# Kernel tuning notes

Hardware: AMD Instinct MI355X
Metric: run time of the kernel (lower is better)

## Reference

```python
import jax, jax.numpy as jnp
import numpy as np

NUM_USERS = 200000
NUM_ITEMS = 200000
D = 64          # embedding_dim
S = 20          # num_sample
N = 100000      # nodes per side
EPS = 1e-12     # torch F.normalize eps


def setup_inputs() -> dict:
    key = jax.random.key(0)
    ks = jax.random.split(key, 14)
    inp = {
        'user_nodes': jax.random.randint(ks[0], (N,), 0, NUM_USERS),
        'item_nodes': jax.random.randint(ks[1], (N,), 0, NUM_ITEMS),
        'user_neighbors': jax.random.randint(ks[2], (N, S), 0, NUM_USERS),
        'item_neighbors': jax.random.randint(ks[3], (N, S), 0, NUM_ITEMS),
        'user_table': 0.01 * jax.random.normal(ks[4], (NUM_USERS, D), jnp.float32),
        'item_table': 0.01 * jax.random.normal(ks[5], (NUM_ITEMS, D), jnp.float32),
        'Wsu': jax.random.normal(ks[6], (D, D), jnp.float32) / np.sqrt(D),
        'bsu': jnp.zeros((D,), jnp.float32),
        'Wnu': jax.random.normal(ks[7], (D, D), jnp.float32) / np.sqrt(D),
        'bnu': jnp.zeros((D,), jnp.float32),
        'Wsi': jax.random.normal(ks[8], (D, D), jnp.float32) / np.sqrt(D),
        'bsi': jnp.zeros((D,), jnp.float32),
        'Wni': jax.random.normal(ks[9], (D, D), jnp.float32) / np.sqrt(D),
        'bni': jnp.zeros((D,), jnp.float32),
    }
    return inp


def _sage_layer(table, nodes, neighbors, Ws, bs, Wn, bn):
    self_e = table[nodes]                        # [N, D] gather
    neigh_agg = jnp.mean(table[neighbors], axis=1)  # [N, S, D] gather -> mean -> [N, D]
    h = jax.nn.relu(self_e @ Ws.T + bs + neigh_agg @ Wn.T + bn)
    # dropout p=0 (eval) -> identity; L2 normalize rows (torch F.normalize)
    norm = jnp.maximum(jnp.linalg.norm(h, axis=1, keepdims=True), EPS)
    return h / norm


def reference(user_nodes, item_nodes, user_neighbors, item_neighbors,
              user_table, item_table,
              Wsu, bsu, Wnu, bnu, Wsi, bsi, Wni, bni):
    user_embs = _sage_layer(user_table, user_nodes, user_neighbors, Wsu, bsu, Wnu, bnu)
    item_embs = _sage_layer(item_table, item_nodes, item_neighbors, Wsi, bsi, Wni, bni)
    return (user_embs, item_embs)
```

## Files before the change

kernel.cpp:

```cpp
#include <hip/hip_runtime.h>

typedef __attribute__((ext_vector_type(8))) short bf16x8;
typedef __attribute__((ext_vector_type(4))) float f32x4;

#define DD 64
#define SS 20
#define NPW 16
#define NPB 64

#define SWZ(u, w) ((((((w) >> 2)) ^ ((u) & 15)) << 2) | ((w) & 3))

__device__ __forceinline__ unsigned cvt_pk_bf16(float lo, float hi) {
    unsigned r;
    asm("v_cvt_pk_bf16_f32 %0, %1, %2" : "=v"(r) : "v"(lo), "v"(hi));
    return r;
}

__global__ __launch_bounds__(256) void to_bf16(const float* __restrict__ src,
                                               uint* __restrict__ dst, long n8)
{
    const long stride = (long)gridDim.x * blockDim.x;
    for (long i = (long)blockIdx.x * blockDim.x + threadIdx.x; i < n8; i += stride) {
        const float4 a = ((const float4*)src)[2 * i];
        const float4 b = ((const float4*)src)[2 * i + 1];
        uint4 p;
        p.x = cvt_pk_bf16(a.x, a.y);
        p.y = cvt_pk_bf16(a.z, a.w);
        p.z = cvt_pk_bf16(b.x, b.y);
        p.w = cvt_pk_bf16(b.z, b.w);
        ((uint4*)dst)[i] = p;
    }
}

__global__ __launch_bounds__(256, 4) void sage_bf16(
    const int*  __restrict__ u_nodes, const int* __restrict__ i_nodes,
    const int*  __restrict__ u_nbrs,  const int* __restrict__ i_nbrs,
    const uint* __restrict__ u_tb,    const uint* __restrict__ i_tb,
    const float* __restrict__ Wsu, const float* __restrict__ bsu,
    const float* __restrict__ Wnu, const float* __restrict__ bnu,
    const float* __restrict__ Wsi, const float* __restrict__ bsi,
    const float* __restrict__ Wni, const float* __restrict__ bni,
    float* __restrict__ out, int N, int nblk_side)
{
    __shared__ unsigned BP[16 * 64 * 4];
    __shared__ unsigned XW[4][NPW][64];

    const int tid    = threadIdx.x;
    const int lane   = tid & 63;
    const int wid    = tid >> 6;
    const int lane15 = lane & 15;
    const int grp    = lane >> 4;

    const bool item_side = (int)blockIdx.x >= nblk_side;
    const int  blk = item_side ? (int)blockIdx.x - nblk_side : (int)blockIdx.x;

    const int*  nodes = item_side ? i_nodes : u_nodes;
    const int*  nbrs  = item_side ? i_nbrs  : u_nbrs;
    const uint* tb    = item_side ? i_tb    : u_tb;
    const float* Ws   = item_side ? Wsi : Wsu;
    const float* bsp  = item_side ? bsi : bsu;
    const float* Wn   = item_side ? Wni : Wnu;
    const float* bnp  = item_side ? bni : bnu;
    float* o = out + (item_side ? (size_t)N * DD : 0);

    #pragma unroll
    for (int it = 0; it < 4; ++it) {
        const int fid = it * 4 + wid;
        const int t = fid >> 2, c = fid & 3;
        const int n  = c * 16 + lane15;
        const int kb = t * 32 + (grp << 3);
        const float* src = (kb < 64) ? (Ws + n * 64 + kb) : (Wn + n * 64 + (kb - 64));
        const float4 v0 = *(const float4*)(src);
        const float4 v1 = *(const float4*)(src + 4);
        uint4 p;
        p.x = cvt_pk_bf16(v0.x, v0.y);
        p.y = cvt_pk_bf16(v0.z, v0.w);
        p.z = cvt_pk_bf16(v1.x, v1.y);
        p.w = cvt_pk_bf16(v1.z, v1.w);
        *(uint4*)&BP[(fid * 64 + lane) * 4] = p;
    }

    float bcol[4];
    #pragma unroll
    for (int c = 0; c < 4; ++c) {
        const int col = c * 16 + lane15;
        bcol[c] = bsp[col] + bnp[col];
    }
    __syncthreads();

    const int n0 = blk * NPB + wid * NPW;
    if (n0 >= N) return;

    const int nd = nodes[min(n0 + lane15, N - 1)];

    #pragma unroll
    for (int sb = 0; sb < 4; ++sb) {
        const int u  = sb * 4 + grp;
        const int nn = min(n0 + u, N - 1);

        const int  nb0 = nbrs[(size_t)nn * SS + lane15];
        const long f1  = min((long)nn * SS + 16 + lane15, (long)N * SS - 1);
        const int  nb1 = nbrs[f1];

        const int sidx = __shfl(nd, u, 64);
        const uint2 sv = ((const uint2*)(tb + (size_t)sidx * 32))[lane15];

        float a0 = 0.f, a1 = 0.f, a2 = 0.f, a3 = 0.f;
        #pragma unroll
        for (int b = 0; b < SS; ++b) {
            const int idx = (b < 16) ? __shfl(nb0, (lane & 48) | b, 64)
                                     : __shfl(nb1, (lane & 48) | (b - 16), 64);
            const uint2 r = ((const uint2*)(tb + (size_t)idx * 32))[lane15];
            a0 += __uint_as_float(r.x << 16);
            a1 += __uint_as_float(r.x & 0xffff0000u);
            a2 += __uint_as_float(r.y << 16);
            a3 += __uint_as_float(r.y & 0xffff0000u);
        }
        const float is = 1.0f / SS;

        const int m = lane15;
        uint2 pagg;
        pagg.x = cvt_pk_bf16(a0 * is, a1 * is);
        pagg.y = cvt_pk_bf16(a2 * is, a3 * is);
        *(uint2*)&XW[wid][u][SWZ(u, 2 * m)]      = sv;
        *(uint2*)&XW[wid][u][SWZ(u, 32 + 2 * m)] = pagg;
    }

    union AB { uint4 u4; bf16x8 v; };
    const f32x4 zero = {0.f, 0.f, 0.f, 0.f};
    f32x4 acc[4] = {zero, zero, zero, zero};
    #pragma unroll
    for (int t = 0; t < 4; ++t) {
        const int r     = lane15;
        const int chunk = t * 4 + grp;
        AB a;
        a.u4 = *(const uint4*)&XW[wid][r][((chunk ^ r) << 2)];
        #pragma unroll
        for (int c = 0; c < 4; ++c) {
            AB b;
            b.u4 = *(const uint4*)&BP[((t * 4 + c) * 64 + lane) * 4];
            acc[c] = __builtin_amdgcn_mfma_f32_16x16x32_bf16(a.v, b.v, acc[c], 0, 0, 0);
        }
    }

    float rl[4][4];
    float ssq[4] = {0.f, 0.f, 0.f, 0.f};
    #pragma unroll
    for (int c = 0; c < 4; ++c) {
        #pragma unroll
        for (int j = 0; j < 4; ++j) {
            const float v = fmaxf(acc[c][j] + bcol[c], 0.f);
            rl[c][j] = v;
            ssq[j] = fmaf(v, v, ssq[j]);
        }
    }
    #pragma unroll
    for (int j = 0; j < 4; ++j) {
        #pragma unroll
        for (int m = 1; m < 16; m <<= 1)
            ssq[j] += __shfl_xor(ssq[j], m, 64);
    }
    float inv[4];
    #pragma unroll
    for (int j = 0; j < 4; ++j)
        inv[j] = 1.0f / fmaxf(sqrtf(ssq[j]), 1e-12f);

    #pragma unroll
    for (int j = 0; j < 4; ++j) {
        const int row = (grp << 2) + j;
        const int ni  = n0 + row;
        if (ni < N) {
            #pragma unroll
            for (int c = 0; c < 4; ++c)
                o[(size_t)ni * DD + c * 16 + lane15] = rl[c][j] * inv[j];
        }
    }
}

__global__ __launch_bounds__(256, 4) void sage_fp32(
    const int*   __restrict__ u_nodes, const int* __restrict__ i_nodes,
    const int*   __restrict__ u_nbrs,  const int* __restrict__ i_nbrs,
    const float* __restrict__ u_table, const float* __restrict__ i_table,
    const float* __restrict__ Wsu, const float* __restrict__ bsu,
    const float* __restrict__ Wnu, const float* __restrict__ bnu,
    const float* __restrict__ Wsi, const float* __restrict__ bsi,
    const float* __restrict__ Wni, const float* __restrict__ bni,
    float* __restrict__ out, int N, int nblk_side)
{
    __shared__ unsigned BP[16 * 64 * 4];
    __shared__ unsigned XW[4][NPW][64];

    const int tid    = threadIdx.x;
    const int lane   = tid & 63;
    const int wid    = tid >> 6;
    const int lane15 = lane & 15;
    const int grp    = lane >> 4;

    const bool item_side = (int)blockIdx.x >= nblk_side;
    const int  blk = item_side ? (int)blockIdx.x - nblk_side : (int)blockIdx.x;

    const int*   nodes = item_side ? i_nodes : u_nodes;
    const int*   nbrs  = item_side ? i_nbrs  : u_nbrs;
    const float* table = item_side ? i_table : u_table;
    const float* Ws    = item_side ? Wsi : Wsu;
    const float* bsp   = item_side ? bsi : bsu;
    const float* Wn    = item_side ? Wni : Wnu;
    const float* bnp   = item_side ? bni : bnu;
    float* o = out + (item_side ? (size_t)N * DD : 0);

    #pragma unroll
    for (int it = 0; it < 4; ++it) {
        const int fid = it * 4 + wid;
        const int t = fid >> 2, c = fid & 3;
        const int n  = c * 16 + lane15;
        const int kb = t * 32 + (grp << 3);
        const float* src = (kb < 64) ? (Ws + n * 64 + kb) : (Wn + n * 64 + (kb - 64));
        const float4 v0 = *(const float4*)(src);
        const float4 v1 = *(const float4*)(src + 4);
        uint4 p;
        p.x = cvt_pk_bf16(v0.x, v0.y);
        p.y = cvt_pk_bf16(v0.z, v0.w);
        p.z = cvt_pk_bf16(v1.x, v1.y);
        p.w = cvt_pk_bf16(v1.z, v1.w);
        *(uint4*)&BP[(fid * 64 + lane) * 4] = p;
    }

    float bcol[4];
    #pragma unroll
    for (int c = 0; c < 4; ++c) bcol[c] = bsp[c * 16 + lane15] + bnp[c * 16 + lane15];
    __syncthreads();

    const int n0 = blk * NPB + wid * NPW;
    if (n0 >= N) return;

    const int nd = nodes[min(n0 + lane15, N - 1)];

    #pragma unroll
    for (int sb = 0; sb < 4; ++sb) {
        const int u  = sb * 4 + grp;
        const int nn = min(n0 + u, N - 1);
        const int  nb0 = nbrs[(size_t)nn * SS + lane15];
        const long f1  = min((long)nn * SS + 16 + lane15, (long)N * SS - 1);
        const int  nb1 = nbrs[f1];
        const int sidx = __shfl(nd, u, 64);
        const float4 self4 = ((const float4*)(table + (size_t)sidx * DD))[lane15];
        float4 agg = {0.f, 0.f, 0.f, 0.f};
        #pragma unroll
        for (int b = 0; b < SS; ++b) {
            const int idx = (b < 16) ? __shfl(nb0, (lane & 48) | b, 64)
                                     : __shfl(nb1, (lane & 48) | (b - 16), 64);
            const float4 r4 = ((const float4*)(table + (size_t)idx * DD))[lane15];
            agg.x += r4.x; agg.y += r4.y; agg.z += r4.z; agg.w += r4.w;
        }
        const float is = 1.0f / SS;
        const int m = lane15;
        uint2 pself, pagg;
        pself.x = cvt_pk_bf16(self4.x, self4.y);
        pself.y = cvt_pk_bf16(self4.z, self4.w);
        pagg.x  = cvt_pk_bf16(agg.x * is, agg.y * is);
        pagg.y  = cvt_pk_bf16(agg.z * is, agg.w * is);
        *(uint2*)&XW[wid][u][SWZ(u, 2 * m)]      = pself;
        *(uint2*)&XW[wid][u][SWZ(u, 32 + 2 * m)] = pagg;
    }

    union AB { uint4 u4; bf16x8 v; };
    const f32x4 zero = {0.f, 0.f, 0.f, 0.f};
    f32x4 acc[4] = {zero, zero, zero, zero};
    #pragma unroll
    for (int t = 0; t < 4; ++t) {
        const int r     = lane15;
        const int chunk = t * 4 + grp;
        AB a;
        a.u4 = *(const uint4*)&XW[wid][r][((chunk ^ r) << 2)];
        #pragma unroll
        for (int c = 0; c < 4; ++c) {
            AB b;
            b.u4 = *(const uint4*)&BP[((t * 4 + c) * 64 + lane) * 4];
            acc[c] = __builtin_amdgcn_mfma_f32_16x16x32_bf16(a.v, b.v, acc[c], 0, 0, 0);
        }
    }

    float rl[4][4];
    float ssq[4] = {0.f, 0.f, 0.f, 0.f};
    #pragma unroll
    for (int c = 0; c < 4; ++c) {
        #pragma unroll
        for (int j = 0; j < 4; ++j) {
            const float v = fmaxf(acc[c][j] + bcol[c], 0.f);
            rl[c][j] = v;
            ssq[j] = fmaf(v, v, ssq[j]);
        }
    }
    #pragma unroll
    for (int j = 0; j < 4; ++j) {
        #pragma unroll
        for (int m = 1; m < 16; m <<= 1) ssq[j] += __shfl_xor(ssq[j], m, 64);
    }
    float inv[4];
    #pragma unroll
    for (int j = 0; j < 4; ++j) inv[j] = 1.0f / fmaxf(sqrtf(ssq[j]), 1e-12f);
    #pragma unroll
    for (int j = 0; j < 4; ++j) {
        const int row = (grp << 2) + j;
        const int ni  = n0 + row;
        if (ni < N) {
            #pragma unroll
            for (int c = 0; c < 4; ++c)
                o[(size_t)ni * DD + c * 16 + lane15] = rl[c][j] * inv[j];
        }
    }
}

extern "C" void kernel_launch(void* const* d_in, const int* in_sizes, int n_in,
                              void* d_out, int out_size, void* d_ws, size_t ws_size,
                              hipStream_t stream) {
    const int*   user_nodes = (const int*)  d_in[0];
    const int*   item_nodes = (const int*)  d_in[1];
    const int*   user_nbrs  = (const int*)  d_in[2];
    const int*   item_nbrs  = (const int*)  d_in[3];
    const float* user_table = (const float*)d_in[4];
    const float* item_table = (const float*)d_in[5];
    const float* Wsu = (const float*)d_in[6];
    const float* bsu = (const float*)d_in[7];
    const float* Wnu = (const float*)d_in[8];
    const float* bnu = (const float*)d_in[9];
    const float* Wsi = (const float*)d_in[10];
    const float* bsi = (const float*)d_in[11];
    const float* Wni = (const float*)d_in[12];
    const float* bni = (const float*)d_in[13];

    float* out = (float*)d_out;
    const int N = in_sizes[0];
    const int nblk_side = (N + NPB - 1) / NPB;

    const long nu = in_sizes[4];
    const long ni = in_sizes[5];
    const size_t need = (size_t)(nu + ni) * 2;

    if (ws_size >= need) {
        uint* u_tb = (uint*)d_ws;
        uint* i_tb = u_tb + (nu >> 1);
        const long nu8 = nu >> 3, ni8 = ni >> 3;
        const int cb = 2048;
        to_bf16<<<cb, 256, 0, stream>>>(user_table, u_tb, nu8);
        to_bf16<<<cb, 256, 0, stream>>>(item_table, i_tb, ni8);
        sage_bf16<<<2 * nblk_side, 256, 0, stream>>>(
            user_nodes, item_nodes, user_nbrs, item_nbrs,
            (const uint*)u_tb, (const uint*)i_tb,
            Wsu, bsu, Wnu, bnu, Wsi, bsi, Wni, bni,
            out, N, nblk_side);
    } else {
        sage_fp32<<<2 * nblk_side, 256, 0, stream>>>(
            user_nodes, item_nodes, user_nbrs, item_nbrs,
            user_table, item_table,
            Wsu, bsu, Wnu, bnu, Wsi, bsi, Wni, bni,
            out, N, nblk_side);
    }
}
```

Measured before the change: 108.9 us.

## Overlap item-table bf16 conversion with user-side SAGE compute in one launch

```diff
diff --git a/kernel.cpp b/kernel.cpp
--- a/kernel.cpp
+++ b/kernel.cpp
@@ -7,6 +7,7 @@
 #define SS 20
 #define NPW 16
 #define NPB 64
+#define CONVB 768
 
 #define SWZ(u, w) ((((((w) >> 2)) ^ ((u) & 15)) << 2) | ((w) & 3))
 
@@ -16,52 +17,59 @@
     return r;
 }
 
-__global__ __launch_bounds__(256) void to_bf16(const float* __restrict__ src,
-                                               uint* __restrict__ dst, long n8)
+__device__ __forceinline__ void conv_body(const float* __restrict__ src,
+                                          uint* __restrict__ dst,
+                                          long n16, long tid0, long stride)
 {
-    const long stride = (long)gridDim.x * blockDim.x;
-    for (long i = (long)blockIdx.x * blockDim.x + threadIdx.x; i < n8; i += stride) {
-        const float4 a = ((const float4*)src)[2 * i];
-        const float4 b = ((const float4*)src)[2 * i + 1];
-        uint4 p;
-        p.x = cvt_pk_bf16(a.x, a.y);
-        p.y = cvt_pk_bf16(a.z, a.w);
-        p.z = cvt_pk_bf16(b.x, b.y);
-        p.w = cvt_pk_bf16(b.z, b.w);
-        ((uint4*)dst)[i] = p;
-    }
-}
-
-__global__ __launch_bounds__(256, 4) void sage_bf16(
-    const int*  __restrict__ u_nodes, const int* __restrict__ i_nodes,
-    const int*  __restrict__ u_nbrs,  const int* __restrict__ i_nbrs,
-    const uint* __restrict__ u_tb,    const uint* __restrict__ i_tb,
-    const float* __restrict__ Wsu, const float* __restrict__ bsu,
-    const float* __restrict__ Wnu, const float* __restrict__ bnu,
-    const float* __restrict__ Wsi, const float* __restrict__ bsi,
-    const float* __restrict__ Wni, const float* __restrict__ bni,
-    float* __restrict__ out, int N, int nblk_side)
+    const float4* s4 = (const float4*)src;
+    uint4* d4 = (uint4*)dst;
+    for (long i = tid0; i < n16; i += stride) {
+        const float4 a = s4[4 * i + 0];
+        const float4 b = s4[4 * i + 1];
+        const float4 c = s4[4 * i + 2];
+        const float4 d = s4[4 * i + 3];
+        uint4 p, q;
+        p.x = cvt_pk_bf16(a.x, a.y);  p.y = cvt_pk_bf16(a.z, a.w);
+        p.z = cvt_pk_bf16(b.x, b.y);  p.w = cvt_pk_bf16(b.z, b.w);
+        q.x = cvt_pk_bf16(c.x, c.y);  q.y = cvt_pk_bf16(c.z, c.w);
+        q.z = cvt_pk_bf16(d.x, d.y);  q.w = cvt_pk_bf16(d.z, d.w);
+        d4[2 * i + 0] = p;
+        d4[2 * i + 1] = q;
+    }
+}
+
+__global__ __launch_bounds__(256) void conv_bf16(const float* __restrict__ src,
+                                                 uint* __restrict__ dst, long n16)
+{
+    conv_body(src, dst, n16,
+              (long)blockIdx.x * blockDim.x + threadIdx.x,
+              (long)gridDim.x * blockDim.x);
+}
+
+__global__ __launch_bounds__(256, 4) void sage_side(
+    const int*  __restrict__ nodes, const int* __restrict__ nbrs,
+    const uint* __restrict__ tb,
+    const float* __restrict__ Ws, const float* __restrict__ bsp,
+    const float* __restrict__ Wn, const float* __restrict__ bnp,
+    float* __restrict__ o, int N,
+    const float* __restrict__ csrc, uint* __restrict__ cdst, long cn16, int convb)
 {
     __shared__ unsigned BP[16 * 64 * 4];
     __shared__ unsigned XW[4][NPW][64];
 
-    const int tid    = threadIdx.x;
+    const int tid = threadIdx.x;
+
+    if ((int)blockIdx.x < convb) {
+        conv_body(csrc, cdst, cn16,
+                  (long)blockIdx.x * 256 + tid, (long)convb * 256);
+        return;
+    }
+    const int blk = (int)blockIdx.x - convb;
+
     const int lane   = tid & 63;
     const int wid    = tid >> 6;
     const int lane15 = lane & 15;
     const int grp    = lane >> 4;
-
-    const bool item_side = (int)blockIdx.x >= nblk_side;
-    const int  blk = item_side ? (int)blockIdx.x - nblk_side : (int)blockIdx.x;
-
-    const int*  nodes = item_side ? i_nodes : u_nodes;
-    const int*  nbrs  = item_side ? i_nbrs  : u_nbrs;
-    const uint* tb    = item_side ? i_tb    : u_tb;
-    const float* Ws   = item_side ? Wsi : Wsu;
-    const float* bsp  = item_side ? bsi : bsu;
-    const float* Wn   = item_side ? Wni : Wnu;
-    const float* bnp  = item_side ? bni : bnu;
-    float* o = out + (item_side ? (size_t)N * DD : 0);
 
     #pragma unroll
     for (int it = 0; it < 4; ++it) {
@@ -340,15 +348,18 @@
     if (ws_size >= need) {
         uint* u_tb = (uint*)d_ws;
         uint* i_tb = u_tb + (nu >> 1);
-        const long nu8 = nu >> 3, ni8 = ni >> 3;
-        const int cb = 2048;
-        to_bf16<<<cb, 256, 0, stream>>>(user_table, u_tb, nu8);
-        to_bf16<<<cb, 256, 0, stream>>>(item_table, i_tb, ni8);
-        sage_bf16<<<2 * nblk_side, 256, 0, stream>>>(
-            user_nodes, item_nodes, user_nbrs, item_nbrs,
-            (const uint*)u_tb, (const uint*)i_tb,
-            Wsu, bsu, Wnu, bnu, Wsi, bsi, Wni, bni,
-            out, N, nblk_side);
+
+        conv_bf16<<<1024, 256, 0, stream>>>(user_table, u_tb, nu >> 4);
+
+        sage_side<<<CONVB + nblk_side, 256, 0, stream>>>(
+            user_nodes, user_nbrs, (const uint*)u_tb,
+            Wsu, bsu, Wnu, bnu, out, N,
+            item_table, i_tb, ni >> 4, CONVB);
+
+        sage_side<<<nblk_side, 256, 0, stream>>>(
+            item_nodes, item_nbrs, (const uint*)i_tb,
+            Wsi, bsi, Wni, bni, out + (size_t)N * DD, N,
+            nullptr, nullptr, 0, 0);
     } else {
         sage_fp32<<<2 * nblk_side, 256, 0, stream>>>(
             user_nodes, item_nodes, user_nbrs, item_nbrs,
```

Measured after the change: 113.9 us. 1.05x slower.
